# Kernel tuning notes

Hardware: AMD Instinct MI355X
Metric: run time of the kernel (lower is better)

## Reference

```python
import jax, jax.numpy as jnp
import numpy as np

B, H, W, C = 8, 128, 128, 128
SCALE = C ** -0.5
EPS = 1e-6  # flax LayerNorm default


def layer_norm(x, scale, bias):
    m = jnp.mean(x, axis=-1, keepdims=True)
    v = jnp.var(x, axis=-1, keepdims=True)
    return (x - m) * jax.lax.rsqrt(v + EPS) * scale + bias


def setup_inputs() -> dict:
    key = jax.random.key(0)
    ks = jax.random.split(key, 12)
    std = 0.02
    return {
        "x_l": jax.random.normal(ks[0], (B, H, W, C), jnp.float32),
        "x_r": jax.random.normal(ks[1], (B, H, W, C), jnp.float32),
        "ln_l_scale": jnp.ones((C,), jnp.float32),
        "ln_l_bias": jnp.zeros((C,), jnp.float32),
        "ln_r_scale": jnp.ones((C,), jnp.float32),
        "ln_r_bias": jnp.zeros((C,), jnp.float32),
        "w_ql": jax.random.normal(ks[2], (C, C), jnp.float32) * std,
        "b_ql": jnp.zeros((C,), jnp.float32),
        "w_qr": jax.random.normal(ks[3], (C, C), jnp.float32) * std,
        "b_qr": jnp.zeros((C,), jnp.float32),
        "w_vl": jax.random.normal(ks[4], (C, C), jnp.float32) * std,
        "b_vl": jnp.zeros((C,), jnp.float32),
        "w_vr": jax.random.normal(ks[5], (C, C), jnp.float32) * std,
        "b_vr": jnp.zeros((C,), jnp.float32),
        "beta": jax.random.normal(ks[6], (1, 1, 1, C), jnp.float32) * std,
        "gamma": jax.random.normal(ks[7], (1, 1, 1, C), jnp.float32) * std,
    }


def reference(x_l, x_r, ln_l_scale, ln_l_bias, ln_r_scale, ln_r_bias,
              w_ql, b_ql, w_qr, b_qr, w_vl, b_vl, w_vr, b_vr, beta, gamma):
    # Q projections of layer-normed inputs  [B,H,W,C]
    q_l = layer_norm(x_l, ln_l_scale, ln_l_bias) @ w_ql + b_ql
    q_r = layer_norm(x_r, ln_r_scale, ln_r_bias) @ w_qr + b_qr
    # V projections of raw inputs
    v_l = x_l @ w_vl + b_vl
    v_r = x_r @ w_vr + b_vr
    # shared cross-view score matrix over the width axis: [B,H,W_l,W_r]
    attention = jnp.einsum('bhic,bhjc->bhij', q_l, q_r) * SCALE
    # dual softmax: rows (axis=-1) and transposed columns
    f_r2l = jnp.einsum('bhij,bhjc->bhic', jax.nn.softmax(attention, axis=-1), v_r) * beta
    f_l2r = jnp.einsum('bhji,bhjc->bhic',
                       jax.nn.softmax(attention, axis=-2), v_l) * gamma
    return (x_l + f_r2l, x_r + f_l2r)
```

## Files before the change

kernel.cpp:

```cpp
#include <hip/hip_runtime.h>


typedef __attribute__((ext_vector_type(8))) __bf16 bf16x8;
typedef __attribute__((ext_vector_type(4))) __bf16 bf16x4;
typedef __attribute__((ext_vector_type(4))) float f4;

#define MFMA(A, B, C) __builtin_amdgcn_mfma_f32_16x16x32_bf16((A), (B), (C), 0, 0, 0)
#define SCALE_QK 0.08838834764831845f

static __device__ __forceinline__ int eoff(int n, int k) {
  return (n << 8) + ((((k >> 3) ^ (n & 7)) << 4) | ((k & 7) << 1));
}

__global__ void prep_w(const float* __restrict__ w0, const float* __restrict__ w1,
                       const float* __restrict__ w2, const float* __restrict__ w3,
                       __bf16* __restrict__ out) {
  int m = blockIdx.y;
  const float* src = (m == 0) ? w0 : (m == 1) ? w1 : (m == 2) ? w2 : w3;
  int t = blockIdx.x * 256 + threadIdx.x;
  int k = t >> 7, n = t & 127;
  out[m * 16384 + n * 128 + k] = (__bf16)src[k * 128 + n];
}

static __device__ __forceinline__ void ln_frags(const float* __restrict__ xp, size_t base,
                                                const float* __restrict__ g,
                                                const float* __restrict__ b, int row,
                                                int quad, bf16x8* lF) {
  float4 v[8];
#pragma unroll
  for (int t = 0; t < 8; ++t)
    v[t] = *(const float4*)(xp + base + row * 128 + (t >> 1) * 32 + quad * 8 + (t & 1) * 4);
  float s = 0.f, s2 = 0.f;
#pragma unroll
  for (int t = 0; t < 8; ++t) {
    s += v[t].x + v[t].y + v[t].z + v[t].w;
    s2 += v[t].x * v[t].x + v[t].y * v[t].y + v[t].z * v[t].z + v[t].w * v[t].w;
  }
  s += __shfl_xor(s, 16);
  s += __shfl_xor(s, 32);
  s2 += __shfl_xor(s2, 16);
  s2 += __shfl_xor(s2, 32);
  float mean = s * 0.0078125f;
  float var = s2 * 0.0078125f - mean * mean;
  float rstd = rsqrtf(var + 1e-6f);
#pragma unroll
  for (int ks = 0; ks < 4; ++ks) {
    bf16x8 lu;
#pragma unroll
    for (int t = 0; t < 2; ++t) {
      float4 q = v[ks * 2 + t];
      float4 gv = *(const float4*)(g + ks * 32 + quad * 8 + t * 4);
      float4 bv = *(const float4*)(b + ks * 32 + quad * 8 + t * 4);
      lu[t * 4 + 0] = (__bf16)((q.x - mean) * rstd * gv.x + bv.x);
      lu[t * 4 + 1] = (__bf16)((q.y - mean) * rstd * gv.y + bv.y);
      lu[t * 4 + 2] = (__bf16)((q.z - mean) * rstd * gv.z + bv.z);
      lu[t * 4 + 3] = (__bf16)((q.w - mean) * rstd * gv.w + bv.w);
    }
    lF[ks] = lu;
  }
}

static __device__ __forceinline__ void x_frags(const float* __restrict__ xp, size_t base,
                                               int row, int quad, bf16x8* xF) {
#pragma unroll 2
  for (int ks = 0; ks < 4; ++ks) {
    bf16x8 xu;
#pragma unroll
    for (int t = 0; t < 2; ++t) {
      float4 q = *(const float4*)(xp + base + row * 128 + ks * 32 + quad * 8 + t * 4);
      xu[t * 4 + 0] = (__bf16)q.x;
      xu[t * 4 + 1] = (__bf16)q.y;
      xu[t * 4 + 2] = (__bf16)q.z;
      xu[t * 4 + 3] = (__bf16)q.w;
    }
    xF[ks] = xu;
  }
}

template <int TRANSPOSED>
static __device__ __forceinline__ void proj_g(const bf16x8* aF,
                                              const __bf16* __restrict__ wTm, char* dst,
                                              const float* __restrict__ bias, float scale,
                                              int w, int l16, int quad) {
#pragma unroll 2
  for (int nt = 0; nt < 8; ++nt) {
    f4 a = {0.f, 0.f, 0.f, 0.f};
    const __bf16* wrow = wTm + (nt * 16 + l16) * 128 + quad * 8;
#pragma unroll
    for (int ks = 0; ks < 4; ++ks) {
      bf16x8 bf = *(const bf16x8*)(wrow + ks * 32);
      a = MFMA(aF[ks], bf, a);
    }
    float bs = bias[nt * 16 + l16];
    if (TRANSPOSED) {
      int c = nt * 16 + l16;
      bf16x4 u;
#pragma unroll
      for (int r = 0; r < 4; ++r) u[r] = (__bf16)((a[r] + bs) * scale);
      *(bf16x4*)(dst + eoff(c, w * 16 + quad * 4)) = u;
    } else {
#pragma unroll
      for (int r = 0; r < 4; ++r) {
        int i = w * 16 + quad * 4 + r;
        *(__bf16*)(dst + eoff(i, nt * 16 + l16)) = (__bf16)((a[r] + bs) * scale);
      }
    }
  }
}

static __device__ __forceinline__ void pv_epi(const bf16x8* pF, const char* vslot,
                                              const float* __restrict__ xp, size_t base,
                                              const float* __restrict__ scl,
                                              float* __restrict__ outp, int w, int l16,
                                              int quad) {
#pragma unroll 2
  for (int nt = 0; nt < 8; ++nt) {
    f4 a = {0.f, 0.f, 0.f, 0.f};
#pragma unroll
    for (int ks = 0; ks < 4; ++ks) {
      bf16x8 bf = *(const bf16x8*)(vslot + eoff(nt * 16 + l16, ks * 32 + quad * 8));
      a = MFMA(pF[ks], bf, a);
    }
    int c = nt * 16 + l16;
    float sv = scl[c];
#pragma unroll
    for (int r = 0; r < 4; ++r) {
      int i = w * 16 + quad * 4 + r;
      outp[base + i * 128 + c] = xp[base + i * 128 + c] + sv * (float)a[r];
    }
  }
}

__global__ __launch_bounds__(512, 4) void scam_fused(
    const float* __restrict__ xl, const float* __restrict__ xr,
    const float* __restrict__ gl, const float* __restrict__ bl,
    const float* __restrict__ gr, const float* __restrict__ br,
    const __bf16* __restrict__ wT,
    const float* __restrict__ bql, const float* __restrict__ bqr,
    const float* __restrict__ bvl, const float* __restrict__ bvr,
    const float* __restrict__ beta, const float* __restrict__ gamma,
    float* __restrict__ out0, float* __restrict__ out1) {
  __shared__ char S[73728];
  char* S1 = S;
  char* S2 = S + 32768;
  float* colred0 = (float*)(S + 65536);
  float* colred1 = (float*)(S + 69632);
  int tid = threadIdx.x;
  int lane = tid & 63, w = tid >> 6;
  int quad = lane >> 4, l16 = lane & 15;
  int row = w * 16 + l16;
  size_t base = (size_t)blockIdx.x << 14;

  {
    bf16x8 llF[4];
    ln_frags(xl, base, gl, bl, row, quad, llF);
    proj_g<0>(llF, wT, S1, bql, SCALE_QK, w, l16, quad);
  }
  {
    bf16x8 lrF[4];
    ln_frags(xr, base, gr, br, row, quad, lrF);
    proj_g<0>(lrF, wT + 16384, S2, bqr, 1.0f, w, l16, quad);
  }
  __syncthreads();

  bf16x8 qlF[4];
#pragma unroll
  for (int ks = 0; ks < 4; ++ks)
    qlF[ks] = *(const bf16x8*)(S1 + eoff(row, ks * 32 + quad * 8));

  f4 sacc[8];
#pragma unroll
  for (int nt = 0; nt < 8; ++nt) {
    f4 z = {0.f, 0.f, 0.f, 0.f};
    sacc[nt] = z;
  }
#pragma unroll
  for (int nt = 0; nt < 8; ++nt)
#pragma unroll
    for (int ks = 0; ks < 4; ++ks) {
      bf16x8 bf = *(const bf16x8*)(S2 + eoff(nt * 16 + l16, ks * 32 + quad * 8));
      sacc[nt] = MFMA(qlF[ks], bf, sacc[nt]);
    }

  {
    float rm[4], rinv[4];
#pragma unroll
    for (int r = 0; r < 4; ++r) {
      float m = -1e30f;
#pragma unroll
      for (int nt = 0; nt < 8; ++nt) m = fmaxf(m, sacc[nt][r]);
#pragma unroll
      for (int d = 1; d < 16; d <<= 1) m = fmaxf(m, __shfl_xor(m, d));
      float s = 0.f;
#pragma unroll
      for (int nt = 0; nt < 8; ++nt) s += __expf(sacc[nt][r] - m);
#pragma unroll
      for (int d = 1; d < 16; d <<= 1) s += __shfl_xor(s, d);
      rm[r] = m;
      rinv[r] = 1.f / s;
    }
#pragma unroll
    for (int nt = 0; nt < 8; ++nt) {
#pragma unroll
      for (int r = 0; r < 4; ++r) {
        int i = w * 16 + quad * 4 + r;
        *(__bf16*)(S1 + eoff(i, nt * 16 + l16)) =
            (__bf16)(__expf(sacc[nt][r] - rm[r]) * rinv[r]);
      }
    }
  }

  float cm[8], cinv[8];
#pragma unroll
  for (int nt = 0; nt < 8; ++nt) {
    float m = fmaxf(fmaxf(sacc[nt][0], sacc[nt][1]), fmaxf(sacc[nt][2], sacc[nt][3]));
    m = fmaxf(m, __shfl_xor(m, 16));
    m = fmaxf(m, __shfl_xor(m, 32));
    float s = __expf(sacc[nt][0] - m) + __expf(sacc[nt][1] - m) +
              __expf(sacc[nt][2] - m) + __expf(sacc[nt][3] - m);
    s += __shfl_xor(s, 16);
    s += __shfl_xor(s, 32);
    cm[nt] = m;
    cinv[nt] = s;
  }
  if (quad == 0) {
#pragma unroll
    for (int nt = 0; nt < 8; ++nt) {
      colred0[w * 128 + nt * 16 + l16] = cm[nt];
      colred1[w * 128 + nt * 16 + l16] = cinv[nt];
    }
  }
  __syncthreads();
#pragma unroll
  for (int nt = 0; nt < 8; ++nt) {
    float m = -1e30f;
#pragma unroll
    for (int ww = 0; ww < 8; ++ww) m = fmaxf(m, colred0[ww * 128 + nt * 16 + l16]);
    float s = 0.f;
#pragma unroll
    for (int ww = 0; ww < 8; ++ww)
      s += colred1[ww * 128 + nt * 16 + l16] *
           __expf(colred0[ww * 128 + nt * 16 + l16] - m);
    cm[nt] = m;
    cinv[nt] = 1.f / s;
  }

#pragma unroll
  for (int nt = 0; nt < 8; ++nt) {
    bf16x4 pc;
#pragma unroll
    for (int r = 0; r < 4; ++r)
      pc[r] = (__bf16)(__expf(sacc[nt][r] - cm[nt]) * cinv[nt]);
    *(bf16x4*)(S2 + eoff(nt * 16 + l16, w * 16 + quad * 4)) = pc;
  }

  bf16x8 xrF[4];
  x_frags(xr, base, row, quad, xrF);

  bf16x8 prF[4];
#pragma unroll
  for (int ks = 0; ks < 4; ++ks)
    prF[ks] = *(const bf16x8*)(S1 + eoff(row, ks * 32 + quad * 8));
  __syncthreads();

  proj_g<1>(xrF, wT + 3 * 16384, S1, bvr, 1.0f, w, l16, quad);
  bf16x8 xlF[4];
  x_frags(xl, base, row, quad, xlF);
  __syncthreads();

  pv_epi(prF, S1, xl, base, beta, out0, w, l16, quad);

  bf16x8 pcF[4];
#pragma unroll
  for (int ks = 0; ks < 4; ++ks)
    pcF[ks] = *(const bf16x8*)(S2 + eoff(row, ks * 32 + quad * 8));
  __syncthreads();

  proj_g<1>(xlF, wT + 2 * 16384, S2, bvl, 1.0f, w, l16, quad);
  __syncthreads();

  pv_epi(pcF, S2, xr, base, gamma, out1, w, l16, quad);
}

extern "C" void kernel_launch(void* const* d_in, const int* in_sizes, int n_in,
                              void* d_out, int out_size, void* d_ws, size_t ws_size,
                              hipStream_t stream) {
  const float* xl = (const float*)d_in[0];
  const float* xr = (const float*)d_in[1];
  const float* gl = (const float*)d_in[2];
  const float* bl = (const float*)d_in[3];
  const float* gr = (const float*)d_in[4];
  const float* br = (const float*)d_in[5];
  const float* wql = (const float*)d_in[6];
  const float* bql = (const float*)d_in[7];
  const float* wqr = (const float*)d_in[8];
  const float* bqr = (const float*)d_in[9];
  const float* wvl = (const float*)d_in[10];
  const float* bvl = (const float*)d_in[11];
  const float* wvr = (const float*)d_in[12];
  const float* bvr = (const float*)d_in[13];
  const float* beta = (const float*)d_in[14];
  const float* gamma = (const float*)d_in[15];

  __bf16* wT = (__bf16*)d_ws;
  float* out0 = (float*)d_out;
  float* out1 = out0 + (size_t)8 * 128 * 128 * 128;

  prep_w<<<dim3(64, 4), 256, 0, stream>>>(wql, wqr, wvl, wvr, wT);
  scam_fused<<<1024, 512, 0, stream>>>(xl, xr, gl, bl, gr, br, wT, bql, bqr, bvl, bvr,
                                       beta, gamma, out0, out1);
}
```

Baseline: 451.7 us.

## Split fused kernel into projection and attention kernels via bf16 workspace

The single fused kernel is split in two. The first kernel computes all four projections (Q and V for both views), writes them as bf16 tiles to a global workspace, and reads each input only once for both layernorm and raw fragments. The second kernel reads Q and V from global memory and does the dual softmax and PV epilogue. This is meant to shorten the serial per-block chain and cut LDS and register pressure, at the cost of an extra round trip of about 128MB of bf16 writes and reads through global memory. The old fused kernel stays as a fallback when the workspace is too small.

```diff
diff --git a/kernel.cpp b/kernel.cpp
--- a/kernel.cpp
+++ b/kernel.cpp
@@ -22,10 +22,10 @@
   out[m * 16384 + n * 128 + k] = (__bf16)src[k * 128 + n];
 }
 
-static __device__ __forceinline__ void ln_frags(const float* __restrict__ xp, size_t base,
-                                                const float* __restrict__ g,
-                                                const float* __restrict__ b, int row,
-                                                int quad, bf16x8* lF) {
+static __device__ __forceinline__ void ln_x_frags(const float* __restrict__ xp,
+                                                  size_t base, const float* __restrict__ g,
+                                                  const float* __restrict__ b, int row,
+                                                  int quad, bf16x8* lF, bf16x8* xF) {
   float4 v[8];
 #pragma unroll
   for (int t = 0; t < 8; ++t)
@@ -45,34 +45,22 @@
   float rstd = rsqrtf(var + 1e-6f);
 #pragma unroll
   for (int ks = 0; ks < 4; ++ks) {
-    bf16x8 lu;
+    bf16x8 lu, xu;
 #pragma unroll
     for (int t = 0; t < 2; ++t) {
       float4 q = v[ks * 2 + t];
       float4 gv = *(const float4*)(g + ks * 32 + quad * 8 + t * 4);
       float4 bv = *(const float4*)(b + ks * 32 + quad * 8 + t * 4);
+      xu[t * 4 + 0] = (__bf16)q.x;
+      xu[t * 4 + 1] = (__bf16)q.y;
+      xu[t * 4 + 2] = (__bf16)q.z;
+      xu[t * 4 + 3] = (__bf16)q.w;
       lu[t * 4 + 0] = (__bf16)((q.x - mean) * rstd * gv.x + bv.x);
       lu[t * 4 + 1] = (__bf16)((q.y - mean) * rstd * gv.y + bv.y);
       lu[t * 4 + 2] = (__bf16)((q.z - mean) * rstd * gv.z + bv.z);
       lu[t * 4 + 3] = (__bf16)((q.w - mean) * rstd * gv.w + bv.w);
     }
     lF[ks] = lu;
-  }
-}
-
-static __device__ __forceinline__ void x_frags(const float* __restrict__ xp, size_t base,
-                                               int row, int quad, bf16x8* xF) {
-#pragma unroll 2
-  for (int ks = 0; ks < 4; ++ks) {
-    bf16x8 xu;
-#pragma unroll
-    for (int t = 0; t < 2; ++t) {
-      float4 q = *(const float4*)(xp + base + row * 128 + ks * 32 + quad * 8 + t * 4);
-      xu[t * 4 + 0] = (__bf16)q.x;
-      xu[t * 4 + 1] = (__bf16)q.y;
-      xu[t * 4 + 2] = (__bf16)q.z;
-      xu[t * 4 + 3] = (__bf16)q.w;
-    }
     xF[ks] = xu;
   }
 }
@@ -108,17 +96,67 @@
   }
 }
 
-static __device__ __forceinline__ void pv_epi(const bf16x8* pF, const char* vslot,
-                                              const float* __restrict__ xp, size_t base,
-                                              const float* __restrict__ scl,
-                                              float* __restrict__ outp, int w, int l16,
-                                              int quad) {
+static __device__ __forceinline__ void copyout(const char* slot, __bf16* __restrict__ dst,
+                                               int tid) {
+#pragma unroll
+  for (int it = 0; it < 4; ++it) {
+    int idx = it * 512 + tid;
+    int n = idx >> 4, seg = idx & 15;
+    *(uint4*)(dst + n * 128 + seg * 8) =
+        *(const uint4*)(slot + (n << 8) + ((seg ^ (n & 7)) << 4));
+  }
+}
+
+__global__ __launch_bounds__(512, 4) void proj4(
+    const float* __restrict__ xl, const float* __restrict__ xr,
+    const float* __restrict__ gl, const float* __restrict__ bl,
+    const float* __restrict__ gr, const float* __restrict__ br,
+    const __bf16* __restrict__ wT, const float* __restrict__ bql,
+    const float* __restrict__ bqr, const float* __restrict__ bvl,
+    const float* __restrict__ bvr, __bf16* __restrict__ qlw,
+    __bf16* __restrict__ qrw, __bf16* __restrict__ vtlw, __bf16* __restrict__ vtrw) {
+  __shared__ char S[65536];
+  char* S1 = S;
+  char* S2 = S + 32768;
+  int tid = threadIdx.x;
+  int lane = tid & 63, w = tid >> 6;
+  int quad = lane >> 4, l16 = lane & 15;
+  int row = w * 16 + l16;
+  size_t base = (size_t)blockIdx.x << 14;
+
+  {
+    bf16x8 lF[4], xF[4];
+    ln_x_frags(xl, base, gl, bl, row, quad, lF, xF);
+    proj_g<0>(lF, wT, S1, bql, SCALE_QK, w, l16, quad);
+    proj_g<1>(xF, wT + 2 * 16384, S2, bvl, 1.0f, w, l16, quad);
+  }
+  __syncthreads();
+  copyout(S1, qlw + base, tid);
+  copyout(S2, vtlw + base, tid);
+  __syncthreads();
+  {
+    bf16x8 lF[4], xF[4];
+    ln_x_frags(xr, base, gr, br, row, quad, lF, xF);
+    proj_g<0>(lF, wT + 16384, S1, bqr, 1.0f, w, l16, quad);
+    proj_g<1>(xF, wT + 3 * 16384, S2, bvr, 1.0f, w, l16, quad);
+  }
+  __syncthreads();
+  copyout(S1, qrw + base, tid);
+  copyout(S2, vtrw + base, tid);
+}
+
+static __device__ __forceinline__ void pv_epi_g(const bf16x8* pF,
+                                                const __bf16* __restrict__ vws,
+                                                const float* __restrict__ xp, size_t base,
+                                                const float* __restrict__ scl,
+                                                float* __restrict__ outp, int w, int l16,
+                                                int quad) {
 #pragma unroll 2
   for (int nt = 0; nt < 8; ++nt) {
     f4 a = {0.f, 0.f, 0.f, 0.f};
 #pragma unroll
     for (int ks = 0; ks < 4; ++ks) {
-      bf16x8 bf = *(const bf16x8*)(vslot + eoff(nt * 16 + l16, ks * 32 + quad * 8));
+      bf16x8 bf = *(const bf16x8*)(vws + (nt * 16 + l16) * 128 + ks * 32 + quad * 8);
       a = MFMA(pF[ks], bf, a);
     }
     int c = nt * 16 + l16;
@@ -131,13 +169,10 @@
   }
 }
 
-__global__ __launch_bounds__(512, 4) void scam_fused(
+__global__ __launch_bounds__(512, 4) void attn2(
     const float* __restrict__ xl, const float* __restrict__ xr,
-    const float* __restrict__ gl, const float* __restrict__ bl,
-    const float* __restrict__ gr, const float* __restrict__ br,
-    const __bf16* __restrict__ wT,
-    const float* __restrict__ bql, const float* __restrict__ bqr,
-    const float* __restrict__ bvl, const float* __restrict__ bvr,
+    const __bf16* __restrict__ qlw, const __bf16* __restrict__ qrw,
+    const __bf16* __restrict__ vtlw, const __bf16* __restrict__ vtrw,
     const float* __restrict__ beta, const float* __restrict__ gamma,
     float* __restrict__ out0, float* __restrict__ out1) {
   __shared__ char S[73728];
@@ -151,22 +186,10 @@
   int row = w * 16 + l16;
   size_t base = (size_t)blockIdx.x << 14;
 
-  {
-    bf16x8 llF[4];
-    ln_frags(xl, base, gl, bl, row, quad, llF);
-    proj_g<0>(llF, wT, S1, bql, SCALE_QK, w, l16, quad);
-  }
-  {
-    bf16x8 lrF[4];
-    ln_frags(xr, base, gr, br, row, quad, lrF);
-    proj_g<0>(lrF, wT + 16384, S2, bqr, 1.0f, w, l16, quad);
-  }
-  __syncthreads();
-
   bf16x8 qlF[4];
 #pragma unroll
   for (int ks = 0; ks < 4; ++ks)
-    qlF[ks] = *(const bf16x8*)(S1 + eoff(row, ks * 32 + quad * 8));
+    qlF[ks] = *(const bf16x8*)(qlw + base + row * 128 + ks * 32 + quad * 8);
 
   f4 sacc[8];
 #pragma unroll
@@ -178,7 +201,8 @@
   for (int nt = 0; nt < 8; ++nt)
 #pragma unroll
     for (int ks = 0; ks < 4; ++ks) {
-      bf16x8 bf = *(const bf16x8*)(S2 + eoff(nt * 16 + l16, ks * 32 + quad * 8));
+      bf16x8 bf =
+          *(const bf16x8*)(qrw + base + (nt * 16 + l16) * 128 + ks * 32 + quad * 8);
       sacc[nt] = MFMA(qlF[ks], bf, sacc[nt]);
     }
 
@@ -210,7 +234,6 @@
     }
   }
 
-  float cm[8], cinv[8];
 #pragma unroll
   for (int nt = 0; nt < 8; ++nt) {
     float m = fmaxf(fmaxf(sacc[nt][0], sacc[nt][1]), fmaxf(sacc[nt][2], sacc[nt][3]));
@@ -220,42 +243,199 @@
               __expf(sacc[nt][2] - m) + __expf(sacc[nt][3] - m);
     s += __shfl_xor(s, 16);
     s += __shfl_xor(s, 32);
-    cm[nt] = m;
-    cinv[nt] = s;
-  }
-  if (quad == 0) {
+    if (quad == 0) {
+      colred0[w * 128 + nt * 16 + l16] = m;
+      colred1[w * 128 + nt * 16 + l16] = s;
+    }
+  }
+  __syncthreads();
+
+#pragma unroll
+  for (int nt = 0; nt < 8; ++nt) {
+    int c = nt * 16 + l16;
+    float m = -1e30f;
+#pragma unroll
+    for (int ww = 0; ww < 8; ++ww) m = fmaxf(m, colred0[ww * 128 + c]);
+    float s = 0.f;
+#pragma unroll
+    for (int ww = 0; ww < 8; ++ww)
+      s += colred1[ww * 128 + c] * __expf(colred0[ww * 128 + c] - m);
+    float inv = 1.f / s;
+    bf16x4 pc;
+#pragma unroll
+    for (int r = 0; r < 4; ++r) pc[r] = (__bf16)(__expf(sacc[nt][r] - m) * inv);
+    *(bf16x4*)(S2 + eoff(c, w * 16 + quad * 4)) = pc;
+  }
+
+  bf16x8 prF[4];
+#pragma unroll
+  for (int ks = 0; ks < 4; ++ks)
+    prF[ks] = *(const bf16x8*)(S1 + eoff(row, ks * 32 + quad * 8));
+  __syncthreads();
+
+  pv_epi_g(prF, vtrw + base, xl, base, beta, out0, w, l16, quad);
+
+  bf16x8 pcF[4];
+#pragma unroll
+  for (int ks = 0; ks < 4; ++ks)
+    pcF[ks] = *(const bf16x8*)(S2 + eoff(row, ks * 32 + quad * 8));
+  pv_epi_g(pcF, vtlw + base, xr, base, gamma, out1, w, l16, quad);
+}
+
+static __device__ __forceinline__ void x_frags(const float* __restrict__ xp, size_t base,
+                                               int row, int quad, bf16x8* xF) {
+#pragma unroll
+  for (int ks = 0; ks < 4; ++ks) {
+    bf16x8 xu;
+#pragma unroll
+    for (int t = 0; t < 2; ++t) {
+      float4 q = *(const float4*)(xp + base + row * 128 + ks * 32 + quad * 8 + t * 4);
+      xu[t * 4 + 0] = (__bf16)q.x;
+      xu[t * 4 + 1] = (__bf16)q.y;
+      xu[t * 4 + 2] = (__bf16)q.z;
+      xu[t * 4 + 3] = (__bf16)q.w;
+    }
+    xF[ks] = xu;
+  }
+}
+
+static __device__ __forceinline__ void pv_epi(const bf16x8* pF, const char* vslot,
+                                              const float* __restrict__ xp, size_t base,
+                                              const float* __restrict__ scl,
+                                              float* __restrict__ outp, int w, int l16,
+                                              int quad) {
+#pragma unroll 2
+  for (int nt = 0; nt < 8; ++nt) {
+    f4 a = {0.f, 0.f, 0.f, 0.f};
+#pragma unroll
+    for (int ks = 0; ks < 4; ++ks) {
+      bf16x8 bf = *(const bf16x8*)(vslot + eoff(nt * 16 + l16, ks * 32 + quad * 8));
+      a = MFMA(pF[ks], bf, a);
+    }
+    int c = nt * 16 + l16;
+    float sv = scl[c];
+#pragma unroll
+    for (int r = 0; r < 4; ++r) {
+      int i = w * 16 + quad * 4 + r;
+      outp[base + i * 128 + c] = xp[base + i * 128 + c] + sv * (float)a[r];
+    }
+  }
+}
+
+__global__ __launch_bounds__(512, 4) void scam_fused(
+    const float* __restrict__ xl, const float* __restrict__ xr,
+    const float* __restrict__ gl, const float* __restrict__ bl,
+    const float* __restrict__ gr, const float* __restrict__ br,
+    const __bf16* __restrict__ wT, const float* __restrict__ bql,
+    const float* __restrict__ bqr, const float* __restrict__ bvl,
+    const float* __restrict__ bvr, const float* __restrict__ beta,
+    const float* __restrict__ gamma, float* __restrict__ out0,
+    float* __restrict__ out1) {
+  __shared__ char S[73728];
+  char* S1 = S;
+  char* S2 = S + 32768;
+  float* colred0 = (float*)(S + 65536);
+  float* colred1 = (float*)(S + 69632);
+  int tid = threadIdx.x;
+  int lane = tid & 63, w = tid >> 6;
+  int quad = lane >> 4, l16 = lane & 15;
+  int row = w * 16 + l16;
+  size_t base = (size_t)blockIdx.x << 14;
+
+  {
+    bf16x8 lF[4], xF[4];
+    ln_x_frags(xl, base, gl, bl, row, quad, lF, xF);
+    proj_g<0>(lF, wT, S1, bql, SCALE_QK, w, l16, quad);
+  }
+  {
+    bf16x8 lF[4], xF[4];
+    ln_x_frags(xr, base, gr, br, row, quad, lF, xF);
+    proj_g<0>(lF, wT + 16384, S2, bqr, 1.0f, w, l16, quad);
+  }
+  __syncthreads();
+
+  bf16x8 qlF[4];
+#pragma unroll
+  for (int ks = 0; ks < 4; ++ks)
+    qlF[ks] = *(const bf16x8*)(S1 + eoff(row, ks * 32 + quad * 8));
+
+  f4 sacc[8];
+#pragma unroll
+  for (int nt = 0; nt < 8; ++nt) {
+    f4 z = {0.f, 0.f, 0.f, 0.f};
+    sacc[nt] = z;
+  }
+#pragma unroll
+  for (int nt = 0; nt < 8; ++nt)
+#pragma unroll
+    for (int ks = 0; ks < 4; ++ks) {
+      bf16x8 bf = *(const bf16x8*)(S2 + eoff(nt * 16 + l16, ks * 32 + quad * 8));
+      sacc[nt] = MFMA(qlF[ks], bf, sacc[nt]);
+    }
+
+  {
+    float rm[4], rinv[4];
+#pragma unroll
+    for (int r = 0; r < 4; ++r) {
+      float m = -1e30f;
+#pragma unroll
+      for (int nt = 0; nt < 8; ++nt) m = fmaxf(m, sacc[nt][r]);
+#pragma unroll
+      for (int d = 1; d < 16; d <<= 1) m = fmaxf(m, __shfl_xor(m, d));
+      float s = 0.f;
+#pragma unroll
+      for (int nt = 0; nt < 8; ++nt) s += __expf(sacc[nt][r] - m);
+#pragma unroll
+      for (int d = 1; d < 16; d <<= 1) s += __shfl_xor(s, d);
+      rm[r] = m;
+      rinv[r] = 1.f / s;
+    }
 #pragma unroll
     for (int nt = 0; nt < 8; ++nt) {
-      colred0[w * 128 + nt * 16 + l16] = cm[nt];
-      colred1[w * 128 + nt * 16 + l16] = cinv[nt];
-    }
-  }
-  __syncthreads();
-#pragma unroll
-  for (int nt = 0; nt < 8; ++nt) {
-    float m = -1e30f;
-#pragma unroll
-    for (int ww = 0; ww < 8; ++ww) m = fmaxf(m, colred0[ww * 128 + nt * 16 + l16]);
-    float s = 0.f;
-#pragma unroll
-    for (int ww = 0; ww < 8; ++ww)
-      s += colred1[ww * 128 + nt * 16 + l16] *
-           __expf(colred0[ww * 128 + nt * 16 + l16] - m);
-    cm[nt] = m;
-    cinv[nt] = 1.f / s;
-  }
-
-#pragma unroll
-  for (int nt = 0; nt < 8; ++nt) {
-    bf16x4 pc;
-#pragma unroll
-    for (int r = 0; r < 4; ++r)
-      pc[r] = (__bf16)(__expf(sacc[nt][r] - cm[nt]) * cinv[nt]);
-    *(bf16x4*)(S2 + eoff(nt * 16 + l16, w * 16 + quad * 4)) = pc;
+#pragma unroll
+      for (int r = 0; r < 4; ++r) {
+        int i = w * 16 + quad * 4 + r;
+        *(__bf16*)(S1 + eoff(i, nt * 16 + l16)) =
+            (__bf16)(__expf(sacc[nt][r] - rm[r]) * rinv[r]);
+      }
+    }
   }
 
   bf16x8 xrF[4];
   x_frags(xr, base, row, quad, xrF);
+
+#pragma unroll
+  for (int nt = 0; nt < 8; ++nt) {
+    float m = fmaxf(fmaxf(sacc[nt][0], sacc[nt][1]), fmaxf(sacc[nt][2], sacc[nt][3]));
+    m = fmaxf(m, __shfl_xor(m, 16));
+    m = fmaxf(m, __shfl_xor(m, 32));
+    float s = __expf(sacc[nt][0] - m) + __expf(sacc[nt][1] - m) +
+              __expf(sacc[nt][2] - m) + __expf(sacc[nt][3] - m);
+    s += __shfl_xor(s, 16);
+    s += __shfl_xor(s, 32);
+    if (quad == 0) {
+      colred0[w * 128 + nt * 16 + l16] = m;
+      colred1[w * 128 + nt * 16 + l16] = s;
+    }
+  }
+  __syncthreads();
+
+#pragma unroll
+  for (int nt = 0; nt < 8; ++nt) {
+    int c = nt * 16 + l16;
+    float m = -1e30f;
+#pragma unroll
+    for (int ww = 0; ww < 8; ++ww) m = fmaxf(m, colred0[ww * 128 + c]);
+    float s = 0.f;
+#pragma unroll
+    for (int ww = 0; ww < 8; ++ww)
+      s += colred1[ww * 128 + c] * __expf(colred0[ww * 128 + c] - m);
+    float inv = 1.f / s;
+    bf16x4 pc;
+#pragma unroll
+    for (int r = 0; r < 4; ++r) pc[r] = (__bf16)(__expf(sacc[nt][r] - m) * inv);
+    *(bf16x4*)(S2 + eoff(c, w * 16 + quad * 4)) = pc;
+  }
 
   bf16x8 prF[4];
 #pragma unroll
@@ -307,6 +487,22 @@
   float* out1 = out0 + (size_t)8 * 128 * 128 * 128;
 
   prep_w<<<dim3(64, 4), 256, 0, stream>>>(wql, wqr, wvl, wvr, wT);
-  scam_fused<<<1024, 512, 0, stream>>>(xl, xr, gl, bl, gr, br, wT, bql, bqr, bvl, bvr,
-                                       beta, gamma, out0, out1);
-}
+
+  const size_t wbytes = 4 * 16384 * sizeof(__bf16);
+  const size_t tile = (size_t)1024 * 16384;
+  const size_t need = wbytes + 4 * tile * sizeof(__bf16);
+
+  if (ws_size >= need) {
+    __bf16* qlw = (__bf16*)((char*)d_ws + wbytes);
+    __bf16* qrw = qlw + tile;
+    __bf16* vtlw = qrw + tile;
+    __bf16* vtrw = vtlw + tile;
+    proj4<<<1024, 512, 0, stream>>>(xl, xr, gl, bl, gr, br, wT, bql, bqr, bvl, bvr,
+                                    qlw, qrw, vtlw, vtrw);
+    attn2<<<1024, 512, 0, stream>>>(xl, xr, qlw, qrw, vtlw, vtrw, beta, gamma, out0,
+                                    out1);
+  } else {
+    scam_fused<<<1024, 512, 0, stream>>>(xl, xr, gl, bl, gr, br, wT, bql, bqr, bvl, bvr,
+                                         beta, gamma, out0, out1);
+  }
+}
```

Measured after the change: 488.0 us. 8.0% more time.
